# Performance work log

Measured on AMD Instinct MI355X. Metric: run time of the kernel, lower is better.

## Reference

```python
import jax, jax.numpy as jnp
import numpy as np

S, B, C = 7, 2, 80
LAMBDA_COORDS = 5.0
LAMBDA_NOOBJ = 0.5


def _iou_cxcywh(a, b):
    """Elementwise IoU of boxes in cx,cy,w,h format, shapes (..., 4) -> (...).
    Same math as torchvision box_convert(cxcywh->xyxy) + box_iou diagonal,
    computed directly (O(S^2)) instead of the O(S^4) pairwise matrix."""
    ax1 = a[..., 0] - a[..., 2] * 0.5
    ay1 = a[..., 1] - a[..., 3] * 0.5
    ax2 = a[..., 0] + a[..., 2] * 0.5
    ay2 = a[..., 1] + a[..., 3] * 0.5
    bx1 = b[..., 0] - b[..., 2] * 0.5
    by1 = b[..., 1] - b[..., 3] * 0.5
    bx2 = b[..., 0] + b[..., 2] * 0.5
    by2 = b[..., 1] + b[..., 3] * 0.5
    inter_w = jnp.clip(jnp.minimum(ax2, bx2) - jnp.maximum(ax1, bx1), 0.0)
    inter_h = jnp.clip(jnp.minimum(ay2, by2) - jnp.maximum(ay1, by1), 0.0)
    inter = inter_w * inter_h
    area_a = (ax2 - ax1) * (ay2 - ay1)
    area_b = (bx2 - bx1) * (by2 - by1)
    return inter / (area_a + area_b - inter)


def setup_inputs() -> dict:
    key = jax.random.key(0)
    k1, k2 = jax.random.split(key)
    N = 8192
    predictions = jax.random.normal(k1, (N, S, S, C + 5 * B), dtype=jnp.float32)
    target = jax.random.uniform(k2, (N, S, S, C + 5), dtype=jnp.float32)
    return {"predictions": predictions, "target": target}


def reference(predictions, target):
    preds = predictions.reshape(-1, S, S, C + 5 * B)
    target_boxes = target[..., -4:]                 # (N,S,S,4)
    pred_boxes_1 = preds[..., -4:]
    pred_boxes_2 = preds[..., -9:-5]

    iou1 = _iou_cxcywh(pred_boxes_1, target_boxes)  # (N,S,S) == diag of box_iou
    iou2 = _iou_cxcywh(pred_boxes_2, target_boxes)
    ious_idx = jnp.argmax(jnp.stack([iou1, iou2], axis=0), axis=0)  # (N,S,S)

    m1 = (1 - ious_idx).astype(preds.dtype)  # responsible-box masks
    m2 = ious_idx.astype(preds.dtype)
    obj = target[..., -5]                    # objectness (N,S,S)

    pred_boxes = obj[..., None] * (m1[..., None] * pred_boxes_1 + m2[..., None] * pred_boxes_2)

    dims = jnp.sign(pred_boxes[..., -2:]) * jnp.sqrt(jnp.abs(pred_boxes[..., -2:]) + 1e-6)
    target_dims = jnp.sqrt(target_boxes[..., -2:])

    sse = lambda a, b: jnp.sum((a - b) ** 2)  # MSELoss(reduction='sum')

    center_loss = sse(pred_boxes[..., :-3], target_boxes[..., :-3]) * LAMBDA_COORDS
    dimensions_loss = sse(dims, target_dims) * LAMBDA_COORDS
    coords_loss = center_loss + dimensions_loss

    obj_pred = preds[..., -5] * m1 + preds[..., -10] * m2
    obj_loss = sse(obj * obj_pred, obj)
    noobj_loss = sse((1.0 - obj) * obj_pred, obj) * LAMBDA_NOOBJ

    classes_loss = sse(preds[..., :-10] * obj[..., None], target[..., :-5])

    return (coords_loss, obj_loss, noobj_loss, classes_loss)
```

## Files before the change

### kernel.cpp

```cpp
#include <hip/hip_runtime.h>
#include <stdint.h>


#define NPRED 90
#define NTGT  85
#define NCLS  80
#define TPB   256
#define NBLK  2048

__device__ __forceinline__ float sgnf(float x) {
    return (x > 0.0f) ? 1.0f : ((x < 0.0f) ? -1.0f : 0.0f);
}

__device__ __forceinline__ float iou_vs_target(
    float acx, float acy, float aw, float ah,
    float bx1, float by1, float bx2, float by2, float area_b)
{
    float ax1 = acx - aw * 0.5f, ay1 = acy - ah * 0.5f;
    float ax2 = acx + aw * 0.5f, ay2 = acy + ah * 0.5f;
    float iw = fmaxf(fminf(ax2, bx2) - fmaxf(ax1, bx1), 0.0f);
    float ih = fmaxf(fminf(ay2, by2) - fmaxf(ay1, by1), 0.0f);
    float inter = iw * ih;
    float area_a = (ax2 - ax1) * (ay2 - ay1);
    return inter / (area_a + area_b - inter);
}

__device__ __forceinline__ void class_quad(
    const float4* __restrict__ pr4, const float* __restrict__ targ,
    long long q, float& clsl)
{
    float4 v = pr4[q];
    unsigned f  = (unsigned)(4ll * q);
    unsigned cl = f / 90u;
    unsigned j  = f - cl * 90u;
    const float* tb = targ + (size_t)cl * NTGT;
    if (j <= 76u) {
        float obj = tb[NCLS];
        float d0 = fmaf(v.x, obj, -tb[j]);
        float d1 = fmaf(v.y, obj, -tb[j + 1]);
        float d2 = fmaf(v.z, obj, -tb[j + 2]);
        float d3 = fmaf(v.w, obj, -tb[j + 3]);
        clsl = fmaf(d0, d0, clsl);
        clsl = fmaf(d1, d1, clsl);
        clsl = fmaf(d2, d2, clsl);
        clsl = fmaf(d3, d3, clsl);
    } else if (j == 78u) {
        float obj = tb[NCLS];
        float d0 = fmaf(v.x, obj, -tb[78]);
        float d1 = fmaf(v.y, obj, -tb[79]);
        clsl = fmaf(d0, d0, clsl);
        clsl = fmaf(d1, d1, clsl);
    } else if (j == 88u) {
        const float* t2 = tb + NTGT;
        float obj2 = t2[NCLS];
        float d0 = fmaf(v.z, obj2, -t2[0]);
        float d1 = fmaf(v.w, obj2, -t2[1]);
        clsl = fmaf(d0, d0, clsl);
        clsl = fmaf(d1, d1, clsl);
    }
}

__global__ __launch_bounds__(TPB, 2) void yolo_loss_kernel(
    const float* __restrict__ preds, const float* __restrict__ targ,
    float* __restrict__ part, float* __restrict__ out,
    int n_cells, int mode)
{
    __shared__ float red[4][4];

    float coords = 0.0f, objl = 0.0f, noobjl = 0.0f, clsl = 0.0f;

    const int tid = threadIdx.x;
    const long long tid0    = (long long)blockIdx.x * TPB + tid;
    const long long tstride = (long long)gridDim.x * TPB;

    const long long n_quads = ((long long)n_cells * NPRED) / 4;
    const float4* pr4 = (const float4*)preds;

    long long q = tid0;
    for (; q + tstride < n_quads; q += 2 * tstride) {
        class_quad(pr4, targ, q,           clsl);
        class_quad(pr4, targ, q + tstride, clsl);
    }
    for (; q < n_quads; q += tstride)
        class_quad(pr4, targ, q, clsl);

    for (long long c = tid0; c < n_cells; c += tstride) {
        const float* pB = preds + (size_t)c * NPRED + NCLS;
        const float* tB = targ  + (size_t)c * NTGT + NCLS;
        float2 b0 = *(const float2*)(pB);
        float2 b1 = *(const float2*)(pB + 2);
        float2 b2 = *(const float2*)(pB + 4);
        float2 b3 = *(const float2*)(pB + 6);
        float2 b4 = *(const float2*)(pB + 8);
        float obj = tB[0];
        float tcx = tB[1], tcy = tB[2], tw = tB[3], th = tB[4];

        float bx1 = tcx - tw * 0.5f, by1 = tcy - th * 0.5f;
        float bx2 = tcx + tw * 0.5f, by2 = tcy + th * 0.5f;
        float area_b = (bx2 - bx1) * (by2 - by1);

        float iou1 = iou_vs_target(b3.x, b3.y, b4.x, b4.y,
                                   bx1, by1, bx2, by2, area_b);
        float iou2 = iou_vs_target(b0.y, b1.x, b1.y, b2.x,
                                   bx1, by1, bx2, by2, area_b);
        bool use2 = iou2 > iou1;

        float pcx = obj * (use2 ? b0.y : b3.x);
        float pw  = obj * (use2 ? b1.y : b4.x);
        float ph  = obj * (use2 ? b2.x : b4.y);

        float dc = pcx - tcx;
        float dw = sgnf(pw) * sqrtf(fabsf(pw) + 1e-6f) - sqrtf(tw);
        float dh = sgnf(ph) * sqrtf(fabsf(ph) + 1e-6f) - sqrtf(th);
        coords = fmaf(dc, dc, coords);
        coords = fmaf(dw, dw, coords);
        coords = fmaf(dh, dh, coords);

        float obj_pred = use2 ? b0.x : b2.y;
        float e1 = fmaf(obj, obj_pred, -obj);
        objl = fmaf(e1, e1, objl);
        float e2 = fmaf(1.0f - obj, obj_pred, -obj);
        noobjl = fmaf(e2, e2, noobjl);
    }

    #pragma unroll
    for (int off = 32; off > 0; off >>= 1) {
        coords += __shfl_down(coords, off);
        objl   += __shfl_down(objl, off);
        noobjl += __shfl_down(noobjl, off);
        clsl   += __shfl_down(clsl, off);
    }

    int wave = tid >> 6;
    int lane = tid & 63;
    if (lane == 0) {
        red[0][wave] = coords;
        red[1][wave] = objl;
        red[2][wave] = noobjl;
        red[3][wave] = clsl;
    }
    __syncthreads();
    if (tid == 0) {
        float c = red[0][0] + red[0][1] + red[0][2] + red[0][3];
        float o = red[1][0] + red[1][1] + red[1][2] + red[1][3];
        float n = red[2][0] + red[2][1] + red[2][2] + red[2][3];
        float k = red[3][0] + red[3][1] + red[3][2] + red[3][3];
        if (mode == 0) {
            int nb = gridDim.x;
            part[0 * nb + blockIdx.x] = c;
            part[1 * nb + blockIdx.x] = o;
            part[2 * nb + blockIdx.x] = n;
            part[3 * nb + blockIdx.x] = k;
        } else {
            atomicAdd(&out[0], 5.0f * c);
            atomicAdd(&out[1], o);
            atomicAdd(&out[2], 0.5f * n);
            atomicAdd(&out[3], k);
        }
    }
}

__global__ __launch_bounds__(256) void yolo_reduce_kernel(
    const float* __restrict__ part, float* __restrict__ out, int nblk)
{
    int w = threadIdx.x >> 6;
    int lane = threadIdx.x & 63;
    float s = 0.0f;
    for (int i = lane; i < nblk; i += 64) s += part[w * nblk + i];
    #pragma unroll
    for (int off = 32; off > 0; off >>= 1) s += __shfl_down(s, off);
    if (lane == 0) {
        float scale = (w == 0) ? 5.0f : (w == 2) ? 0.5f : 1.0f;
        out[w] = s * scale;
    }
}

extern "C" void kernel_launch(void* const* d_in, const int* in_sizes, int n_in,
                              void* d_out, int out_size, void* d_ws, size_t ws_size,
                              hipStream_t stream) {
    const float* preds = (const float*)d_in[0];
    const float* targ  = (const float*)d_in[1];
    float* out = (float*)d_out;

    int n_cells = in_sizes[0] / NPRED;

    bool use_ws = ws_size >= (size_t)(4 * NBLK) * sizeof(float);

    if (use_ws) {
        float* part = (float*)d_ws;
        hipLaunchKernelGGL(yolo_loss_kernel, dim3(NBLK), dim3(TPB), 0, stream,
                           preds, targ, part, out, n_cells, 0);
        hipLaunchKernelGGL(yolo_reduce_kernel, dim3(1), dim3(256), 0, stream,
                           part, out, NBLK);
        if (out_size > 4) {
            hipMemsetAsync(out + 4, 0, (size_t)(out_size - 4) * sizeof(float), stream);
        }
    } else {
        hipMemsetAsync(d_out, 0, (size_t)out_size * sizeof(float), stream);
        hipLaunchKernelGGL(yolo_loss_kernel, dim3(NBLK), dim3(TPB), 0, stream,
                           preds, targ, (float*)nullptr, out, n_cells, 1);
    }
}
```

Baseline: 309.0 us.

## Fuse box-loss computation into the class streaming pass via wave shuffles

Removes the second per-cell loop that re-read the 10 box fields of every prediction with strided loads. Box losses are now computed inside the vectorised class pass: the thread whose quad starts at offset 80 or 78 gathers the neighbouring quads with __shfl_down, and falls back to global loads at wave edges. Prediction loads also become non-temporal. The loop now only processes whole 64-quad wave chunks, so it drops any tail when n_quads is not a multiple of 64. It also adds divergent branches and shuffles on every iteration.

```diff
diff --git a/kernel.cpp b/kernel.cpp
--- a/kernel.cpp
+++ b/kernel.cpp
@@ -7,6 +7,8 @@
 #define NCLS  80
 #define TPB   256
 #define NBLK  2048
+
+typedef float vfloat4 __attribute__((ext_vector_type(4)));
 
 __device__ __forceinline__ float sgnf(float x) {
     return (x > 0.0f) ? 1.0f : ((x < 0.0f) ? -1.0f : 0.0f);
@@ -25,15 +27,55 @@
     return inter / (area_a + area_b - inter);
 }
 
-__device__ __forceinline__ void class_quad(
-    const float4* __restrict__ pr4, const float* __restrict__ targ,
-    long long q, float& clsl)
-{
-    float4 v = pr4[q];
+__device__ __forceinline__ void box_loss(
+    float pb0, float pb1, float pb2, float pb3, float pb4,
+    float pb5, float pb6, float pb7, float pb8, float pb9,
+    const float* __restrict__ tb,
+    float& coords, float& objl, float& noobjl)
+{
+    float obj = tb[NCLS];
+    float tcx = tb[81], tcy = tb[82], tw = tb[83], th = tb[84];
+    float bx1 = tcx - tw * 0.5f, by1 = tcy - th * 0.5f;
+    float bx2 = tcx + tw * 0.5f, by2 = tcy + th * 0.5f;
+    float area_b = (bx2 - bx1) * (by2 - by1);
+
+    float iou1 = iou_vs_target(pb6, pb7, pb8, pb9, bx1, by1, bx2, by2, area_b);
+    float iou2 = iou_vs_target(pb1, pb2, pb3, pb4, bx1, by1, bx2, by2, area_b);
+    bool use2 = iou2 > iou1;
+
+    float pcx = obj * (use2 ? pb1 : pb6);
+    float pw  = obj * (use2 ? pb3 : pb8);
+    float ph  = obj * (use2 ? pb4 : pb9);
+
+    float dc = pcx - tcx;
+    float dw = sgnf(pw) * sqrtf(fabsf(pw) + 1e-6f) - sqrtf(tw);
+    float dh = sgnf(ph) * sqrtf(fabsf(ph) + 1e-6f) - sqrtf(th);
+    coords = fmaf(dc, dc, coords);
+    coords = fmaf(dw, dw, coords);
+    coords = fmaf(dh, dh, coords);
+
+    float obj_pred = use2 ? pb0 : pb5;
+    float e1 = fmaf(obj, obj_pred, -obj);
+    objl = fmaf(e1, e1, objl);
+    float e2 = fmaf(1.0f - obj, obj_pred, -obj);
+    noobjl = fmaf(e2, e2, noobjl);
+}
+
+__device__ __forceinline__ void handle_quad(
+    vfloat4 v, long long q, int lane,
+    const float* __restrict__ preds, const float* __restrict__ targ,
+    float& clsl, float& coords, float& objl, float& noobjl)
+{
+    float s1x = __shfl_down(v.x, 1), s1y = __shfl_down(v.y, 1);
+    float s1z = __shfl_down(v.z, 1), s1w = __shfl_down(v.w, 1);
+    float s2x = __shfl_down(v.x, 2), s2y = __shfl_down(v.y, 2);
+    float s2z = __shfl_down(v.z, 2), s2w = __shfl_down(v.w, 2);
+
     unsigned f  = (unsigned)(4ll * q);
     unsigned cl = f / 90u;
     unsigned j  = f - cl * 90u;
     const float* tb = targ + (size_t)cl * NTGT;
+
     if (j <= 76u) {
         float obj = tb[NCLS];
         float d0 = fmaf(v.x, obj, -tb[j]);
@@ -58,6 +100,28 @@
         clsl = fmaf(d0, d0, clsl);
         clsl = fmaf(d1, d1, clsl);
     }
+
+    if (j == 80u) {
+        if (lane < 62) {
+            box_loss(v.x, v.y, v.z, v.w, s1x, s1y, s1z, s1w, s2x, s2y,
+                     tb, coords, objl, noobjl);
+        } else {
+            const float* pB = preds + (size_t)cl * NPRED + NCLS;
+            box_loss(pB[0], pB[1], pB[2], pB[3], pB[4],
+                     pB[5], pB[6], pB[7], pB[8], pB[9],
+                     tb, coords, objl, noobjl);
+        }
+    } else if (j == 78u) {
+        if (lane < 62) {
+            box_loss(v.z, v.w, s1x, s1y, s1z, s1w, s2x, s2y, s2z, s2w,
+                     tb, coords, objl, noobjl);
+        } else {
+            const float* pB = preds + (size_t)cl * NPRED + NCLS;
+            box_loss(pB[0], pB[1], pB[2], pB[3], pB[4],
+                     pB[5], pB[6], pB[7], pB[8], pB[9],
+                     tb, coords, objl, noobjl);
+        }
+    }
 }
 
 __global__ __launch_bounds__(TPB, 2) void yolo_loss_kernel(
@@ -69,58 +133,27 @@
 
     float coords = 0.0f, objl = 0.0f, noobjl = 0.0f, clsl = 0.0f;
 
-    const int tid = threadIdx.x;
-    const long long tid0    = (long long)blockIdx.x * TPB + tid;
+    const int tid  = threadIdx.x;
+    const int lane = tid & 63;
+
+    const long long n_quads = ((long long)n_cells * NPRED) / 4;
     const long long tstride = (long long)gridDim.x * TPB;
-
-    const long long n_quads = ((long long)n_cells * NPRED) / 4;
-    const float4* pr4 = (const float4*)preds;
-
-    long long q = tid0;
-    for (; q + tstride < n_quads; q += 2 * tstride) {
-        class_quad(pr4, targ, q,           clsl);
-        class_quad(pr4, targ, q + tstride, clsl);
-    }
-    for (; q < n_quads; q += tstride)
-        class_quad(pr4, targ, q, clsl);
-
-    for (long long c = tid0; c < n_cells; c += tstride) {
-        const float* pB = preds + (size_t)c * NPRED + NCLS;
-        const float* tB = targ  + (size_t)c * NTGT + NCLS;
-        float2 b0 = *(const float2*)(pB);
-        float2 b1 = *(const float2*)(pB + 2);
-        float2 b2 = *(const float2*)(pB + 4);
-        float2 b3 = *(const float2*)(pB + 6);
-        float2 b4 = *(const float2*)(pB + 8);
-        float obj = tB[0];
-        float tcx = tB[1], tcy = tB[2], tw = tB[3], th = tB[4];
-
-        float bx1 = tcx - tw * 0.5f, by1 = tcy - th * 0.5f;
-        float bx2 = tcx + tw * 0.5f, by2 = tcy + th * 0.5f;
-        float area_b = (bx2 - bx1) * (by2 - by1);
-
-        float iou1 = iou_vs_target(b3.x, b3.y, b4.x, b4.y,
-                                   bx1, by1, bx2, by2, area_b);
-        float iou2 = iou_vs_target(b0.y, b1.x, b1.y, b2.x,
-                                   bx1, by1, bx2, by2, area_b);
-        bool use2 = iou2 > iou1;
-
-        float pcx = obj * (use2 ? b0.y : b3.x);
-        float pw  = obj * (use2 ? b1.y : b4.x);
-        float ph  = obj * (use2 ? b2.x : b4.y);
-
-        float dc = pcx - tcx;
-        float dw = sgnf(pw) * sqrtf(fabsf(pw) + 1e-6f) - sqrtf(tw);
-        float dh = sgnf(ph) * sqrtf(fabsf(ph) + 1e-6f) - sqrtf(th);
-        coords = fmaf(dc, dc, coords);
-        coords = fmaf(dw, dw, coords);
-        coords = fmaf(dh, dh, coords);
-
-        float obj_pred = use2 ? b0.x : b2.y;
-        float e1 = fmaf(obj, obj_pred, -obj);
-        objl = fmaf(e1, e1, objl);
-        float e2 = fmaf(1.0f - obj, obj_pred, -obj);
-        noobjl = fmaf(e2, e2, noobjl);
+    const vfloat4* pr4 = (const vfloat4*)preds;
+
+    long long wb = (long long)blockIdx.x * TPB + (long long)(tid & ~63);
+
+    for (; wb + tstride + 64 <= n_quads; wb += 2 * tstride) {
+        vfloat4 va = __builtin_nontemporal_load(pr4 + wb + lane);
+        vfloat4 vc = __builtin_nontemporal_load(pr4 + wb + tstride + lane);
+        handle_quad(va, wb + lane,           lane, preds, targ,
+                    clsl, coords, objl, noobjl);
+        handle_quad(vc, wb + tstride + lane, lane, preds, targ,
+                    clsl, coords, objl, noobjl);
+    }
+    for (; wb + 64 <= n_quads; wb += tstride) {
+        vfloat4 va = __builtin_nontemporal_load(pr4 + wb + lane);
+        handle_quad(va, wb + lane, lane, preds, targ,
+                    clsl, coords, objl, noobjl);
     }
 
     #pragma unroll
@@ -132,7 +165,6 @@
     }
 
     int wave = tid >> 6;
-    int lane = tid & 63;
     if (lane == 0) {
         red[0][wave] = coords;
         red[1][wave] = objl;
```

Result: slower. 354.8 us (+14.8%).
